# Optimization experiments

Measured on AMD Instinct MI355X. Metric: run time of the kernel, lower is better.

The kernel has to match this reference:

```python
import jax, jax.numpy as jnp
import numpy as np

H = 97
IN = 9
N_NODES = 100000
N_EDGES = 800000
N_GRAPHS = 4096
N_LAYERS = 7
N_STEPS = 7
BN_EPS = 1e-5


def setup_inputs() -> dict:
    key = jax.random.key(0)
    ks = iter(jax.random.split(key, 40))
    sc = 0.1  # param init scale
    inp = {}
    inp['x'] = jax.random.normal(next(ks), (N_NODES, IN), jnp.float32)
    inp['edge_index'] = jax.random.randint(next(ks), (2, N_EDGES), 0, N_NODES, jnp.int32)
    inp['batch'] = jnp.sort(jax.random.randint(next(ks), (N_NODES,), 0, N_GRAPHS, jnp.int32))
    inp['num_graphs'] = N_GRAPHS
    inp['lin1_W'] = jax.random.normal(next(ks), (IN, H), jnp.float32) * sc
    inp['lin1_b'] = jax.random.normal(next(ks), (H,), jnp.float32) * sc
    for nm in ['Wk', 'Wq', 'Wv', 'Ws']:
        inp['conv_' + nm] = jax.random.normal(next(ks), (N_LAYERS, H, H), jnp.float32) * sc
    for nm in ['bk', 'bq', 'bv', 'bs']:
        inp['conv_' + nm] = jax.random.normal(next(ks), (N_LAYERS, H), jnp.float32) * sc
    inp['gru_Wih'] = jax.random.normal(next(ks), (N_LAYERS, H, 3 * H), jnp.float32) * sc
    inp['gru_Whh'] = jax.random.normal(next(ks), (N_LAYERS, H, 3 * H), jnp.float32) * sc
    inp['gru_bih'] = jax.random.normal(next(ks), (N_LAYERS, 3 * H), jnp.float32) * sc
    inp['gru_bhh'] = jax.random.normal(next(ks), (N_LAYERS, 3 * H), jnp.float32) * sc
    inp['bn_gamma'] = jnp.ones((N_LAYERS - 1, H), jnp.float32)
    inp['bn_beta'] = jnp.zeros((N_LAYERS - 1, H), jnp.float32)
    inp['bn_mean'] = jnp.zeros((N_LAYERS - 1, H), jnp.float32)
    inp['bn_var'] = jnp.ones((N_LAYERS - 1, H), jnp.float32)
    inp['gat_W'] = jax.random.normal(next(ks), (H, H), jnp.float32) * sc
    inp['gat_asrc'] = jax.random.normal(next(ks), (H,), jnp.float32) * sc
    inp['gat_adst'] = jax.random.normal(next(ks), (H,), jnp.float32) * sc
    inp['gat_b'] = jax.random.normal(next(ks), (H,), jnp.float32) * sc
    inp['molgru_Wih'] = jax.random.normal(next(ks), (H, 3 * H), jnp.float32) * sc
    inp['molgru_Whh'] = jax.random.normal(next(ks), (H, 3 * H), jnp.float32) * sc
    inp['molgru_bih'] = jax.random.normal(next(ks), (3 * H,), jnp.float32) * sc
    inp['molgru_bhh'] = jax.random.normal(next(ks), (3 * H,), jnp.float32) * sc
    inp['lin2_W'] = jax.random.normal(next(ks), (H, 1), jnp.float32) * sc
    inp['lin2_b'] = jax.random.normal(next(ks), (1,), jnp.float32) * sc
    return inp


def _gru(xin, h, Wih, Whh, bih, bhh):
    gi = xin @ Wih + bih  # [N, 3H]
    gh = h @ Whh + bhh
    ir, iz, inn = jnp.split(gi, 3, axis=-1)
    hr, hz, hn = jnp.split(gh, 3, axis=-1)
    r = jax.nn.sigmoid(ir + hr)
    z = jax.nn.sigmoid(iz + hz)
    n = jnp.tanh(inn + r * hn)
    return (1.0 - z) * n + z * h


def _resgated(x, src, dst, Wk, bk, Wq, bq, Wv, bv, Ws, bs, n_nodes):
    # PyG ResGatedGraphConv: out_i = Ws x_i + sum_j sigmoid(Wk x_i + Wq x_j) * (Wv x_j)
    k = x @ Wk + bk
    q = x @ Wq + bq
    v = x @ Wv + bv
    msg = jax.nn.sigmoid(k[dst] + q[src]) * v[src]  # [E, H]
    agg = jax.ops.segment_sum(msg, dst, num_segments=n_nodes)
    return agg + (x @ Ws + bs)


def _forward(x, lin1_W, lin1_b, conv_Wk, conv_bk, conv_Wq, conv_bq, conv_Wv, conv_bv,
             conv_Ws, conv_bs, gru_Wih, gru_Whh, gru_bih, gru_bhh,
             bn_gamma, bn_beta, bn_mean, bn_var,
             gat_W, gat_asrc, gat_adst, gat_b,
             molgru_Wih, molgru_Whh, molgru_bih, molgru_bhh,
             lin2_W, lin2_b, edge_index, batch, num_graphs):
    src, dst = edge_index[0], edge_index[1]
    n_nodes = x.shape[0]
    x = jax.nn.leaky_relu(x @ lin1_W + lin1_b, 0.01)
    # layer 0 (gate_conv + gru)
    h = jax.nn.elu(_resgated(x, src, dst, conv_Wk[0], conv_bk[0], conv_Wq[0], conv_bq[0],
                             conv_Wv[0], conv_bv[0], conv_Ws[0], conv_bs[0], n_nodes))
    x = jax.nn.relu(_gru(h, x, gru_Wih[0], gru_Whh[0], gru_bih[0], gru_bhh[0]))
    # layers 1..6 with eval-mode BatchNorm (dropout inactive in eval)
    for l in range(1, N_LAYERS):
        h = jax.nn.elu(_resgated(x, src, dst, conv_Wk[l], conv_bk[l], conv_Wq[l], conv_bq[l],
                                 conv_Wv[l], conv_bv[l], conv_Ws[l], conv_bs[l], n_nodes))
        b = l - 1
        h = (h - bn_mean[b]) * (bn_gamma[b] / jnp.sqrt(bn_var[b] + BN_EPS)) + bn_beta[b]
        x = jax.nn.relu(_gru(h, x, gru_Wih[l], gru_Whh[l], gru_bih[l], gru_bhh[l]))
    # molecule readout: global_add_pool then bipartite GAT (heads=1) over node->graph edges
    out = jax.nn.relu(jax.ops.segment_sum(x, batch, num_segments=num_graphs))  # [G, H]
    xs = x @ gat_W          # source projections, fixed over timesteps
    a_s = xs @ gat_asrc     # [N]
    for _ in range(N_STEPS):
        a_d = (out @ gat_W) @ gat_adst  # [G]
        alpha = jax.nn.leaky_relu(a_s + a_d[batch], 0.01)  # one score per node-edge
        m = jax.ops.segment_max(alpha, batch, num_segments=num_graphs)
        m = jnp.where(jnp.isfinite(m), m, 0.0)
        e = jnp.exp(alpha - m[batch])
        s = jax.ops.segment_sum(e, batch, num_segments=num_graphs)
        w = e / s[batch]  # segment softmax over each graph's nodes
        hg = jax.ops.segment_sum(w[:, None] * xs, batch, num_segments=num_graphs) + gat_b
        h = jax.nn.elu(hg)
        out = jax.nn.relu(_gru(h, out, molgru_Wih, molgru_Whh, molgru_bih, molgru_bhh))
    return out @ lin2_W + lin2_b  # [G, 1]


def reference(x, edge_index, batch, num_graphs, lin1_W, lin1_b, conv_Wk, conv_bk, conv_Wq,
              conv_bq, conv_Wv, conv_bv, conv_Ws, conv_bs, gru_Wih, gru_Whh, gru_bih, gru_bhh,
              bn_gamma, bn_beta, bn_mean, bn_var, gat_W, gat_asrc, gat_adst, gat_b,
              molgru_Wih, molgru_Whh, molgru_bih, molgru_bhh, lin2_W, lin2_b):
    return _forward(x, lin1_W, lin1_b, conv_Wk, conv_bk, conv_Wq, conv_bq, conv_Wv, conv_bv,
                    conv_Ws, conv_bs, gru_Wih, gru_Whh, gru_bih, gru_bhh,
                    bn_gamma, bn_beta, bn_mean, bn_var,
                    gat_W, gat_asrc, gat_adst, gat_b,
                    molgru_Wih, molgru_Whh, molgru_bih, molgru_bhh,
                    lin2_W, lin2_b, edge_index, batch, num_graphs)
```

## Files before the change

kernel.cpp:

```cpp
#include <hip/hip_runtime.h>

#define NN 100000
#define NNP 100032
#define NE 800000
#define NG 4096
#define HH 97
#define HP 128
#define NB 391

typedef unsigned short u16;
typedef unsigned int u32;
typedef __attribute__((ext_vector_type(8))) short short8v;
typedef __attribute__((ext_vector_type(4))) float f32x4;

__device__ __forceinline__ float sigm_(float x){ return 1.f/(1.f+__expf(-x)); }
__device__ __forceinline__ float lrelu01_(float x){ return x>0.f? x : 0.01f*x; }
__device__ __forceinline__ float tanh_(float t){ float e2=__expf(2.f*t); return 1.f-2.f/(e2+1.f); }
__device__ __forceinline__ float b2f(u16 u){ union{u32 i; float f;} t; t.i=(u32)u<<16; return t.f; }
__device__ __forceinline__ u16 f2b(float x){ union{float f; u32 i;} t; t.f=x; u32 r=t.i+0x7FFFu+((t.i>>16)&1u); return (u16)(r>>16); }

__device__ __forceinline__ f32x4 mfma16(short8v a, short8v b, f32x4 c){
  return __builtin_amdgcn_mfma_f32_16x16x32_bf16(a, b, c, 0, 0, 0);
}

__global__ void k_pack_convw(const float* __restrict__ Wk, const float* __restrict__ Wq,
                             const float* __restrict__ Wv, const float* __restrict__ Ws,
                             u16* __restrict__ out){
  int idx = blockIdx.x*256 + threadIdx.x;
  if (idx >= 7*2*4*32*512) return;
  int e = idx & 7, lane = (idx>>3) & 63, t = (idx>>9) & 31;
  int ks = (idx>>14) & 3, term = (idx>>16) & 1, l = idx>>17;
  int k = ks*32 + (lane>>4)*8 + e;
  int n = t*16 + (lane & 15);
  int m = n>>7, h = n & 127;
  float val = 0.f;
  if (k < HH && h < HH){
    const float* W = (m==0)? Wk : (m==1)? Wq : (m==2)? Wv : Ws;
    val = W[l*9409 + k*97 + h];
  }
  u16 hi = f2b(val);
  out[idx] = (term==0)? hi : f2b(val - b2f(hi));
}

__global__ void k_pack_gruw(const float* __restrict__ gih, const float* __restrict__ ghh,
                            const float* __restrict__ mih, const float* __restrict__ mhh,
                            u16* __restrict__ out){
  int idx = blockIdx.x*256 + threadIdx.x;
  if (idx >= 8*2*2*4*24*512) return;
  int e = idx & 7, lane = (idx>>3) & 63;
  int r1 = idx>>9;
  int t = r1 % 24, r2 = r1 / 24;
  int ks = r2 & 3, mt = (r2>>2) & 3, set = r2>>4;
  int mat = mt>>1, term = mt & 1;
  int k = ks*32 + (lane>>4)*8 + e;
  int n = t*16 + (lane & 15);
  int j = n>>7, g = n & 127;
  float val = 0.f;
  if (k < HH && g < HH){
    const float* src = (set < 7)? ((mat==0)? gih + (size_t)set*28227 : ghh + (size_t)set*28227)
                                : ((mat==0)? mih : mhh);
    val = src[k*291 + j*97 + g];
  }
  u16 hi = f2b(val);
  out[idx] = (term==0)? hi : f2b(val - b2f(hi));
}

__global__ void k_pack_gatw(const float* __restrict__ gatW, u16* __restrict__ out){
  int idx = blockIdx.x*256 + threadIdx.x;
  if (idx >= 2*4*8*512) return;
  int e = idx & 7, lane = (idx>>3) & 63, t = (idx>>9) & 7;
  int ks = (idx>>12) & 3, term = idx>>14;
  int k = ks*32 + (lane>>4)*8 + e;
  int h = t*16 + (lane & 15);
  float val = (k < HH && h < HH)? gatW[k*97 + h] : 0.f;
  u16 hi = f2b(val);
  out[idx] = (term==0)? hi : f2b(val - b2f(hi));
}

__global__ void k_pack_w96(const float* __restrict__ Wk, const float* __restrict__ Wq,
                           const float* __restrict__ Wv, const float* __restrict__ Ws,
                           const float* __restrict__ gih, const float* __restrict__ ghh,
                           const float* __restrict__ mih, const float* __restrict__ mhh,
                           float* __restrict__ out){
  int idx = blockIdx.x*256 + threadIdx.x;
  if (idx < 7*512){
    int l = idx >> 9, c = idx & 511;
    int m = c >> 7, h = c & 127;
    float v = 0.f;
    if (h < HH){
      const float* W = (m==0)? Wk : (m==1)? Wq : (m==2)? Wv : Ws;
      v = W[l*9409 + 96*97 + h];
    }
    out[idx] = v;
  } else if (idx < 7*512 + 8*384){
    int r = idx - 7*512;
    int set = r / 384, n = r % 384;
    int j = n >> 7, g = n & 127;
    float v = 0.f;
    if (g < HH){
      const float* srcp = (set < 7)? gih + (size_t)set*28227 : mih;
      v = srcp[96*291 + j*97 + g];
    }
    out[idx] = v;
  } else if (idx < 7*512 + 16*384){
    int r = idx - 7*512 - 8*384;
    int set = r / 384, n = r % 384;
    int j = n >> 7, g = n & 127;
    float v = 0.f;
    if (g < HH){
      const float* srcp = (set < 7)? ghh + (size_t)set*28227 : mhh;
      v = srcp[96*291 + j*97 + g];
    }
    out[idx] = v;
  }
}

__global__ void k_pack_convb(const float* __restrict__ bk, const float* __restrict__ bq,
                             const float* __restrict__ bv, const float* __restrict__ bs,
                             float* __restrict__ out){
  int idx = blockIdx.x*256 + threadIdx.x;
  if (idx >= 7*512) return;
  int l = idx >> 9, c = idx & 511;
  int m = c >> 7, h = c & 127;
  float v = 0.f;
  if (h < HH){
    const float* B = (m==0)? bk : (m==1)? bq : (m==2)? bv : bs;
    v = B[l*97 + h];
  }
  out[idx] = v;
}

__global__ void k_pack_grub(const float* __restrict__ gbi, const float* __restrict__ gbh,
                            const float* __restrict__ mbi, const float* __restrict__ mbh,
                            float* __restrict__ obi, float* __restrict__ obh){
  int idx = blockIdx.x*256 + threadIdx.x;
  if (idx >= 8*384) return;
  int set = idx / 384, n = idx % 384;
  int j = n>>7, g = n & 127;
  float vi = 0.f, vh = 0.f;
  if (g < HH){
    const float* si = (set < 7)? gbi + set*291 : mbi;
    const float* sh = (set < 7)? gbh + set*291 : mbh;
    vi = si[j*97 + g];
    vh = sh[j*97 + g];
  }
  obi[idx] = vi; obh[idx] = vh;
}

__global__ void k_pack_misc(const float* __restrict__ gatW, const float* __restrict__ asrc,
                            const float* __restrict__ adst, const float* __restrict__ gatb,
                            const float* __restrict__ l2W, float* __restrict__ out){
  int idx = blockIdx.x*256 + threadIdx.x;
  if (idx < 16384){
    int k = idx >> 7, h = idx & 127;
    out[idx] = (k < HH && h < HH)? gatW[k*97 + h] : 0.f;
  } else if (idx < 16512){
    int h = idx - 16384; out[idx] = (h < HH)? asrc[h] : 0.f;
  } else if (idx < 16640){
    int h = idx - 16512; out[idx] = (h < HH)? adst[h] : 0.f;
  } else if (idx < 16768){
    int h = idx - 16640; out[idx] = (h < HH)? gatb[h] : 0.f;
  } else if (idx < 16896){
    int h = idx - 16768; out[idx] = (h < HH)? l2W[h] : 0.f;
  } else if (idx < 17408){
    out[idx] = 0.f;
  }
}

__global__ void k_seg(const int* __restrict__ batch, int* __restrict__ seg){
  int g = blockIdx.x*blockDim.x + threadIdx.x;
  if (g > NG) return;
  int lo = 0, hi = NN;
  while (lo < hi){ int mid = (lo+hi) >> 1; if (batch[mid] < g) lo = mid+1; else hi = mid; }
  seg[g] = lo;
}

__global__ void k_hist(const int* __restrict__ dst, int* __restrict__ cnt){
  int e = blockIdx.x*256 + threadIdx.x;
  if (e < NE) atomicAdd(&cnt[dst[e]], 1);
}

__global__ void k_scan_blk(const int* __restrict__ cnt, int* __restrict__ offs,
                           int* __restrict__ bsum){
  __shared__ int s[256];
  int b = blockIdx.x, t = threadIdx.x, i = b*256 + t;
  int v = (i < NN)? cnt[i] : 0;
  s[t] = v; __syncthreads();
  #pragma unroll
  for (int off = 1; off < 256; off <<= 1){
    int tmp = (t >= off)? s[t-off] : 0;
    __syncthreads();
    s[t] += tmp;
    __syncthreads();
  }
  if (i < NN) offs[i] = s[t] - v;
  if (t == 255) bsum[b] = s[255];
}

__global__ void k_scan_top(int* __restrict__ bsum){
  __shared__ int s[512];
  int t = threadIdx.x;
  int v = (t < NB)? bsum[t] : 0;
  s[t] = v; __syncthreads();
  #pragma unroll
  for (int off = 1; off < 512; off <<= 1){
    int tmp = (t >= off)? s[t-off] : 0;
    __syncthreads();
    s[t] += tmp;
    __syncthreads();
  }
  if (t < NB) bsum[t] = s[t] - v;
}

__global__ void k_scan_add(int* __restrict__ offs, const int* __restrict__ bsum,
                           int* __restrict__ cur){
  int b = blockIdx.x, t = threadIdx.x, i = b*256 + t;
  if (i < NN){ int o = offs[i] + bsum[b]; offs[i] = o; cur[i] = o; }
  if (i == 0) offs[NN] = NE;
}

__global__ void k_scatter(const int* __restrict__ src, const int* __restrict__ dst,
                          int* __restrict__ cur, int* __restrict__ eidx){
  int e = blockIdx.x*256 + threadIdx.x;
  if (e >= NE) return;
  int pos = atomicAdd(&cur[dst[e]], 1);
  eidx[pos] = src[e];
}

__global__ __launch_bounds__(256) void k_lin1(const float* __restrict__ x,
    const float* __restrict__ W, const float* __restrict__ b, u16* __restrict__ X0){
  int idx = blockIdx.x*256 + threadIdx.x;
  int n = idx >> 7, c = idx & 127;
  float v = 0.f;
  if (n < NN && c < HH){
    v = b[c];
    #pragma unroll
    for (int k = 0; k < 9; ++k) v += x[n*9 + k]*W[k*HH + c];
    v = lrelu01_(v);
  }
  X0[(size_t)n*HP + c] = f2b(v);
}

__global__ __launch_bounds__(256) void k_conv_mfma(const u16* __restrict__ X,
    const u16* __restrict__ WCF_l, const float* __restrict__ biasp,
    const float* __restrict__ W96C, u16* __restrict__ KQV, float* __restrict__ S){
  int tid = threadIdx.x;
  int w = tid >> 6, lane = tid & 63;
  int lm = lane & 15, ls = lane >> 4;
  int m0 = blockIdx.x*64;
  f32x4 acc[4][8] = {};
  for (int ks = 0; ks < 3; ++ks){
    short8v aX[4];
    #pragma unroll
    for (int rb = 0; rb < 4; ++rb)
      aX[rb] = *(const short8v*)(X + (size_t)(m0 + rb*16 + lm)*HP + ks*32 + ls*8);
    short8v wf[8][2];
    #pragma unroll
    for (int t = 0; t < 8; ++t){
      int tg = w*8 + t;
      wf[t][0] = *(const short8v*)(WCF_l + (((size_t)(0*4 + ks)*32 + tg)*64 + lane)*8);
      wf[t][1] = *(const short8v*)(WCF_l + (((size_t)(1*4 + ks)*32 + tg)*64 + lane)*8);
    }
    #pragma unroll
    for (int t = 0; t < 8; ++t)
      #pragma unroll
      for (int rb = 0; rb < 4; ++rb){
        acc[rb][t] = mfma16(aX[rb], wf[t][0], acc[rb][t]);
        acc[rb][t] = mfma16(aX[rb], wf[t][1], acc[rb][t]);
      }
  }
  float x96[4][4];
  #pragma unroll
  for (int rb = 0; rb < 4; ++rb)
    #pragma unroll
    for (int r = 0; r < 4; ++r)
      x96[rb][r] = b2f(X[(size_t)(m0 + rb*16 + ls*4 + r)*HP + 96]);
  #pragma unroll
  for (int t = 0; t < 8; ++t){
    int c = t*16 + lm;
    int col = w*128 + c;
    float bv = biasp[col];
    float w96 = W96C[col];
    #pragma unroll
    for (int rb = 0; rb < 4; ++rb)
      #pragma unroll
      for (int r = 0; r < 4; ++r){
        int row = m0 + rb*16 + ls*4 + r;
        float v = acc[rb][t][r] + bv + x96[rb][r]*w96;
        if (w < 3) KQV[(size_t)row*384 + w*128 + c] = f2b(v);
        else       S[(size_t)row*HP + c] = v;
      }
  }
}

__global__ __launch_bounds__(256) void k_gru_mfma(const float* __restrict__ Hin,
    const u16* __restrict__ Xin, const u16* __restrict__ WGF_set,
    const float* __restrict__ bihp, const float* __restrict__ bhhp,
    const float* __restrict__ W96I, const float* __restrict__ W96H,
    u16* __restrict__ Xout){
  int tid = threadIdx.x;
  int w = tid >> 6, lane = tid & 63;
  int lm = lane & 15, ls = lane >> 4;
  int m0 = blockIdx.x*32;
  f32x4 agi[2][2][3] = {};
  f32x4 agh[2][2][3] = {};
  for (int ks = 0; ks < 3; ++ks){
    short8v aX[2], aSh[2], aSl[2];
    #pragma unroll
    for (int rb = 0; rb < 2; ++rb){
      int row = m0 + rb*16 + lm;
      aX[rb] = *(const short8v*)(Xin + (size_t)row*HP + ks*32 + ls*8);
      const float* sp = Hin + (size_t)row*HP + ks*32 + ls*8;
      float sv[8];
      *(float4*)&sv[0] = *(const float4*)sp;
      *(float4*)&sv[4] = *(const float4*)(sp + 4);
      short8v vh, vl;
      #pragma unroll
      for (int e = 0; e < 8; ++e){
        u16 hb = f2b(sv[e]);
        vh[e] = (short)hb;
        vl[e] = (short)f2b(sv[e] - b2f(hb));
      }
      aSh[rb] = vh; aSl[rb] = vl;
    }
    #pragma unroll
    for (int b = 0; b < 2; ++b){
      short8v fI[3][2], fH[3][2];
      #pragma unroll
      for (int j = 0; j < 3; ++j){
        int t = j*8 + 2*w + b;
        fI[j][0] = *(const short8v*)(WGF_set + (((size_t)(0*4 + ks)*24 + t)*64 + lane)*8);
        fI[j][1] = *(const short8v*)(WGF_set + (((size_t)(1*4 + ks)*24 + t)*64 + lane)*8);
        fH[j][0] = *(const short8v*)(WGF_set + (((size_t)(2*4 + ks)*24 + t)*64 + lane)*8);
        fH[j][1] = *(const short8v*)(WGF_set + (((size_t)(3*4 + ks)*24 + t)*64 + lane)*8);
      }
      #pragma unroll
      for (int j = 0; j < 3; ++j)
        #pragma unroll
        for (int rb = 0; rb < 2; ++rb){
          agi[rb][b][j] = mfma16(aSh[rb], fI[j][0], agi[rb][b][j]);
          agi[rb][b][j] = mfma16(aSh[rb], fI[j][1], agi[rb][b][j]);
          agi[rb][b][j] = mfma16(aSl[rb], fI[j][0], agi[rb][b][j]);
          agh[rb][b][j] = mfma16(aX[rb], fH[j][0], agh[rb][b][j]);
          agh[rb][b][j] = mfma16(aX[rb], fH[j][1], agh[rb][b][j]);
        }
    }
  }
  float s96[2][4], x96[2][4];
  #pragma unroll
  for (int rb = 0; rb < 2; ++rb)
    #pragma unroll
    for (int r = 0; r < 4; ++r){
      int row = m0 + rb*16 + ls*4 + r;
      s96[rb][r] = Hin[(size_t)row*HP + 96];
      x96[rb][r] = b2f(Xin[(size_t)row*HP + 96]);
    }
  #pragma unroll
  for (int b = 0; b < 2; ++b){
    int g = (2*w + b)*16 + lm;
    float bi0 = bihp[g], bi1 = bihp[128+g], bi2 = bihp[256+g];
    float bh0 = bhhp[g], bh1 = bhhp[128+g], bh2 = bhhp[256+g];
    float wi0 = W96I[g], wi1 = W96I[128+g], wi2 = W96I[256+g];
    float wh0 = W96H[g], wh1 = W96H[128+g], wh2 = W96H[256+g];
    #pragma unroll
    for (int rb = 0; rb < 2; ++rb)
      #pragma unroll
      for (int r = 0; r < 4; ++r){
        int row = m0 + rb*16 + ls*4 + r;
        float ir = agi[rb][b][0][r] + bi0 + s96[rb][r]*wi0;
        float iz = agi[rb][b][1][r] + bi1 + s96[rb][r]*wi1;
        float in_ = agi[rb][b][2][r] + bi2 + s96[rb][r]*wi2;
        float hr = agh[rb][b][0][r] + bh0 + x96[rb][r]*wh0;
        float hz = agh[rb][b][1][r] + bh1 + x96[rb][r]*wh1;
        float hn = agh[rb][b][2][r] + bh2 + x96[rb][r]*wh2;
        float rr = sigm_(ir + hr);
        float zz = sigm_(iz + hz);
        float nn2 = tanh_(in_ + rr*hn);
        float xo = b2f(Xin[(size_t)row*HP + g]);
        float v = (1.f - zz)*nn2 + zz*xo;
        Xout[(size_t)row*HP + g] = f2b(fmaxf(v, 0.f));
      }
  }
}

__global__ __launch_bounds__(256) void k_xs_mfma(const u16* __restrict__ X,
    const u16* __restrict__ GATF, u16* __restrict__ XS){
  int tid = threadIdx.x;
  int w = tid >> 6, lane = tid & 63;
  int lm = lane & 15, ls = lane >> 4;
  int m0 = blockIdx.x*32;
  f32x4 acc[2][2] = {};
  for (int ks = 0; ks < 4; ++ks){
    short8v aX[2];
    #pragma unroll
    for (int rb = 0; rb < 2; ++rb){
      int row = m0 + rb*16 + lm;
      aX[rb] = *(const short8v*)(X + (size_t)row*HP + ks*32 + ls*8);
    }
    #pragma unroll
    for (int b = 0; b < 2; ++b){
      int t = 2*w + b;
      short8v bh = *(const short8v*)(GATF + (((size_t)(0*4 + ks)*8 + t)*64 + lane)*8);
      short8v bl = *(const short8v*)(GATF + (((size_t)(1*4 + ks)*8 + t)*64 + lane)*8);
      #pragma unroll
      for (int rb = 0; rb < 2; ++rb){
        acc[rb][b] = mfma16(aX[rb], bh, acc[rb][b]);
        acc[rb][b] = mfma16(aX[rb], bl, acc[rb][b]);
      }
    }
  }
  #pragma unroll
  for (int b = 0; b < 2; ++b){
    int c = (2*w + b)*16 + lm;
    #pragma unroll
    for (int rb = 0; rb < 2; ++rb)
      #pragma unroll
      for (int r = 0; r < 4; ++r){
        int row = m0 + rb*16 + ls*4 + r;
        XS[(size_t)row*HP + c] = f2b(acc[rb][b][r]);
      }
  }
}

__global__ __launch_bounds__(256) void k_agg(const u16* __restrict__ kqv,
    const int* __restrict__ offs, const int* __restrict__ eidx,
    float* __restrict__ S, const float* __restrict__ gamma, const float* __restrict__ beta,
    const float* __restrict__ mean, const float* __restrict__ var, int layer){
  int n = blockIdx.x*4 + (threadIdx.x >> 6);
  if (n >= NN) return;
  int lane = threadIdx.x & 63;
  int c2 = lane*2;
  int lo = offs[n], hi = offs[n+1];
  ushort2 kk = *(const ushort2*)(kqv + (size_t)n*384 + c2);
  float k0 = b2f(kk.x), k1 = b2f(kk.y);
  float a0 = 0.f, a1 = 0.f;
  int i = lo;
  for (; i + 4 <= hi; i += 4){
    int s0 = eidx[i], s1 = eidx[i+1], s2 = eidx[i+2], s3 = eidx[i+3];
    const u16* q0 = kqv + (size_t)s0*384 + 128 + c2;
    const u16* q1 = kqv + (size_t)s1*384 + 128 + c2;
    const u16* q2 = kqv + (size_t)s2*384 + 128 + c2;
    const u16* q3 = kqv + (size_t)s3*384 + 128 + c2;
    ushort2 qa = *(const ushort2*)q0, va = *(const ushort2*)(q0 + 128);
    ushort2 qb = *(const ushort2*)q1, vb = *(const ushort2*)(q1 + 128);
    ushort2 qc = *(const ushort2*)q2, vc = *(const ushort2*)(q2 + 128);
    ushort2 qd = *(const ushort2*)q3, vd = *(const ushort2*)(q3 + 128);
    a0 += b2f(va.x)*sigm_(k0 + b2f(qa.x)); a1 += b2f(va.y)*sigm_(k1 + b2f(qa.y));
    a0 += b2f(vb.x)*sigm_(k0 + b2f(qb.x)); a1 += b2f(vb.y)*sigm_(k1 + b2f(qb.y));
    a0 += b2f(vc.x)*sigm_(k0 + b2f(qc.x)); a1 += b2f(vc.y)*sigm_(k1 + b2f(qc.y));
    a0 += b2f(vd.x)*sigm_(k0 + b2f(qd.x)); a1 += b2f(vd.y)*sigm_(k1 + b2f(qd.y));
  }
  for (; i < hi; ++i){
    int s = eidx[i];
    const u16* qb0 = kqv + (size_t)s*384 + 128 + c2;
    ushort2 qq = *(const ushort2*)qb0;
    ushort2 vv = *(const ushort2*)(qb0 + 128);
    a0 += b2f(vv.x)*sigm_(k0 + b2f(qq.x));
    a1 += b2f(vv.y)*sigm_(k1 + b2f(qq.y));
  }
  float* sp = S + (size_t)n*HP + c2;
  float2 sr = *(float2*)sp;
  float v0 = sr.x + a0, v1 = sr.y + a1;
  v0 = v0 > 0.f ? v0 : (__expf(v0) - 1.f);
  v1 = v1 > 0.f ? v1 : (__expf(v1) - 1.f);
  if (layer > 0){
    int b0 = (layer-1)*97 + c2;
    if (c2 < HH){ float sc = gamma[b0]*rsqrtf(var[b0] + 1e-5f); v0 = (v0 - mean[b0])*sc + beta[b0]; }
    if (c2+1 < HH){ float sc = gamma[b0+1]*rsqrtf(var[b0+1] + 1e-5f); v1 = (v1 - mean[b0+1])*sc + beta[b0+1]; }
  }
  if (c2 >= HH)   v0 = 0.f;
  if (c2+1 >= HH) v1 = 0.f;
  *(float2*)sp = make_float2(v0, v1);
}

__global__ __launch_bounds__(128) void k_pool(const int* __restrict__ seg,
    const u16* __restrict__ x, u16* __restrict__ out){
  int g = blockIdx.x, tid = threadIdx.x;
  int lo = seg[g], hi = seg[g+1];
  float acc = 0.f;
  for (int n = lo; n < hi; ++n) acc += b2f(x[(size_t)n*HP + tid]);
  out[(size_t)g*HP + tid] = f2b(fmaxf(acc, 0.f));
}

__global__ __launch_bounds__(256) void k_as(const u16* __restrict__ xs,
    const float* __restrict__ asrcp, float* __restrict__ a_s){
  int t = blockIdx.x*256 + threadIdx.x;
  int n = t >> 6, lane = t & 63;
  float v = b2f(xs[(size_t)n*HP + lane])*asrcp[lane]
          + b2f(xs[(size_t)n*HP + 64 + lane])*asrcp[64 + lane];
  #pragma unroll
  for (int o = 32; o > 0; o >>= 1) v += __shfl_down(v, o);
  if (lane == 0) a_s[n] = v;
}

__global__ __launch_bounds__(128) void k_ad(const u16* __restrict__ out,
    const float* __restrict__ gatwp, const float* __restrict__ adstp, float* __restrict__ ad){
  int g = blockIdx.x, tid = threadIdx.x;
  __shared__ float so[HP];
  __shared__ float red[2];
  so[tid] = b2f(out[(size_t)g*HP + tid]);
  __syncthreads();
  float p = 0.f;
  #pragma unroll 4
  for (int k = 0; k < HP; ++k) p += so[k]*gatwp[k*HP + tid];
  float v = p * adstp[tid];
  #pragma unroll
  for (int o = 32; o > 0; o >>= 1) v += __shfl_down(v, o);
  if ((tid & 63) == 0) red[tid >> 6] = v;
  __syncthreads();
  if (tid == 0) ad[g] = red[0] + red[1];
}

#define ACAP 2048
__global__ __launch_bounds__(128) void k_attn(const int* __restrict__ seg,
    const float* __restrict__ a_s, const float* __restrict__ a_d,
    const u16* __restrict__ xs, const float* __restrict__ gbp, float* __restrict__ hg){
  int g = blockIdx.x, tid = threadIdx.x;
  int lo = seg[g], hi = seg[g+1], cnt = hi - lo;
  float ad = a_d[g];
  __shared__ float sa[ACAP];
  __shared__ float red[2];
  float mloc = -3.4e38f;
  for (int i = tid; i < cnt; i += 128){
    float al = lrelu01_(a_s[lo+i] + ad);
    if (i < ACAP) sa[i] = al;
    mloc = fmaxf(mloc, al);
  }
  #pragma unroll
  for (int o = 32; o > 0; o >>= 1) mloc = fmaxf(mloc, __shfl_down(mloc, o));
  if ((tid & 63) == 0) red[tid >> 6] = mloc;
  __syncthreads();
  float mm = fmaxf(red[0], red[1]);
  __syncthreads();
  float sloc = 0.f;
  for (int i = tid; i < cnt; i += 128){
    float al = (i < ACAP)? sa[i] : lrelu01_(a_s[lo+i] + ad);
    float e = __expf(al - mm);
    if (i < ACAP) sa[i] = e;
    sloc += e;
  }
  #pragma unroll
  for (int o = 32; o > 0; o >>= 1) sloc += __shfl_down(sloc, o);
  if ((tid & 63) == 0) red[tid >> 6] = sloc;
  __syncthreads();
  float ss = red[0] + red[1];
  float inv = (cnt > 0 && ss != 0.f)? 1.f/ss : 0.f;
  __syncthreads();
  float accv = 0.f;
  for (int i = 0; i < cnt; ++i){
    float e = (i < ACAP)? sa[i] : __expf(lrelu01_(a_s[lo+i] + ad) - mm);
    accv += (e*inv) * b2f(xs[(size_t)(lo+i)*HP + tid]);
  }
  float hgv = accv + gbp[tid];
  hg[(size_t)g*HP + tid] = hgv > 0.f ? hgv : (__expf(hgv) - 1.f);
}

__global__ __launch_bounds__(64) void k_final(const u16* __restrict__ out,
    const float* __restrict__ w2p, const float* __restrict__ l2b, float* __restrict__ y){
  int g = blockIdx.x, lane = threadIdx.x;
  float v = b2f(out[(size_t)g*HP + lane])*w2p[lane]
          + b2f(out[(size_t)g*HP + 64 + lane])*w2p[64 + lane];
  #pragma unroll
  for (int o = 32; o > 0; o >>= 1) v += __shfl_down(v, o);
  if (lane == 0) y[g] = v + l2b[0];
}

extern "C" void kernel_launch(void* const* d_in, const int* in_sizes, int n_in,
                              void* d_out, int out_size, void* d_ws, size_t ws_size,
                              hipStream_t stream){
  const float* x_in  = (const float*)d_in[0];
  const int*   ei    = (const int*)d_in[1];
  const int*   batch = (const int*)d_in[2];
  const float* lin1W = (const float*)d_in[4];
  const float* lin1b = (const float*)d_in[5];
  const float* cWk = (const float*)d_in[6];
  const float* cWq = (const float*)d_in[7];
  const float* cWv = (const float*)d_in[8];
  const float* cWs = (const float*)d_in[9];
  const float* cbk = (const float*)d_in[10];
  const float* cbq = (const float*)d_in[11];
  const float* cbv = (const float*)d_in[12];
  const float* cbs = (const float*)d_in[13];
  const float* gWih = (const float*)d_in[14];
  const float* gWhh = (const float*)d_in[15];
  const float* gbih = (const float*)d_in[16];
  const float* gbhh = (const float*)d_in[17];
  const float* bng = (const float*)d_in[18];
  const float* bnb = (const float*)d_in[19];
  const float* bnm = (const float*)d_in[20];
  const float* bnv = (const float*)d_in[21];
  const float* gatW  = (const float*)d_in[22];
  const float* gasrc = (const float*)d_in[23];
  const float* gadst = (const float*)d_in[24];
  const float* gatb  = (const float*)d_in[25];
  const float* mWih = (const float*)d_in[26];
  const float* mWhh = (const float*)d_in[27];
  const float* mbih = (const float*)d_in[28];
  const float* mbhh = (const float*)d_in[29];
  const float* l2W = (const float*)d_in[30];
  const float* l2b = (const float*)d_in[31];
  const int* src = ei;
  const int* dst = ei + NE;

  char* base = (char*)d_ws;
  size_t off = 0;
  auto alloc = [&](size_t nbytes)->char*{
    char* p = base + off; off = (off + nbytes + 255) & ~(size_t)255; return p; };

  u16*  WCF  = (u16*)alloc((size_t)7*2*4*32*512*2);
  u16*  WGF  = (u16*)alloc((size_t)8*2*2*4*24*512*2);
  u16*  GATF = (u16*)alloc((size_t)2*4*8*512*2);
  float* W96  = (float*)alloc((size_t)(7*512 + 16*384)*4);
  float* BCONVP = (float*)alloc(7*512*4);
  float* BIHP   = (float*)alloc(8*384*4);
  float* BHHP   = (float*)alloc(8*384*4);
  float* GATWP  = (float*)alloc(17408*4);
  float* ASRCP = GATWP + 16384;
  float* ADSTP = GATWP + 16512;
  float* GBP   = GATWP + 16640;
  float* W2P   = GATWP + 16768;
  u16*  X0  = (u16*)alloc((size_t)NNP*HP*2);
  u16*  X1  = (u16*)alloc((size_t)NNP*HP*2);
  u16*  KQV = (u16*)alloc((size_t)NNP*384*2);
  float* S  = (float*)alloc((size_t)NNP*HP*4);
  float* AS_ = (float*)alloc((size_t)NN*4);
  float* AD_ = (float*)alloc((size_t)NG*4);
  u16*  OUTA = (u16*)alloc((size_t)NG*HP*2);
  u16*  OUTB = (u16*)alloc((size_t)NG*HP*2);
  float* HG  = (float*)alloc((size_t)NG*HP*4);
  int*  SEG  = (int*)alloc((size_t)(NG+1)*4);
  int*  CNT  = (int*)alloc((size_t)NN*4);
  int*  OFFS = (int*)alloc((size_t)(NN+1)*4);
  int*  CUR  = (int*)alloc((size_t)NN*4);
  int*  EIDX = (int*)alloc((size_t)NE*4);
  int*  BSUM = (int*)alloc((size_t)NB*4);

  float* W96C = W96;
  float* W96I = W96 + 7*512;
  float* W96H = W96 + 7*512 + 8*384;

  if (ws_size < off){
    hipMemsetAsync(d_out, 0, (size_t)out_size*sizeof(float), stream);
    return;
  }

  k_pack_convw<<<(7*2*4*32*512+255)/256,256,0,stream>>>(cWk,cWq,cWv,cWs,WCF);
  k_pack_gruw<<<(8*2*2*4*24*512+255)/256,256,0,stream>>>(gWih,gWhh,mWih,mWhh,WGF);
  k_pack_gatw<<<(2*4*8*512+255)/256,256,0,stream>>>(gatW,GATF);
  k_pack_w96<<<(7*512+16*384+255)/256,256,0,stream>>>(cWk,cWq,cWv,cWs,gWih,gWhh,mWih,mWhh,W96);
  k_pack_convb<<<(7*512+255)/256,256,0,stream>>>(cbk,cbq,cbv,cbs,BCONVP);
  k_pack_grub<<<(8*384+255)/256,256,0,stream>>>(gbih,gbhh,mbih,mbhh,BIHP,BHHP);
  k_pack_misc<<<68,256,0,stream>>>(gatW,gasrc,gadst,gatb,l2W,GATWP);
  k_lin1<<<(NNP*HP)/256,256,0,stream>>>(x_in,lin1W,lin1b,X0);
  k_seg<<<(NG+1+255)/256,256,0,stream>>>(batch,SEG);

  hipMemsetAsync(CNT, 0, (size_t)NN*4, stream);
  k_hist<<<(NE+255)/256,256,0,stream>>>(dst, CNT);
  k_scan_blk<<<NB,256,0,stream>>>(CNT, OFFS, BSUM);
  k_scan_top<<<1,512,0,stream>>>(BSUM);
  k_scan_add<<<NB,256,0,stream>>>(OFFS, BSUM, CUR);
  k_scatter<<<(NE+255)/256,256,0,stream>>>(src, dst, CUR, EIDX);

  for (int l = 0; l < 7; ++l){
    u16* Xin  = (l & 1)? X1 : X0;
    u16* Xout = (l & 1)? X0 : X1;
    k_conv_mfma<<<NNP/64,256,0,stream>>>(Xin, WCF + (size_t)l*131072, BCONVP + l*512,
                                         W96C + l*512, KQV, S);
    k_agg<<<(NN+3)/4,256,0,stream>>>(KQV, OFFS, EIDX, S, bng, bnb, bnm, bnv, l);
    k_gru_mfma<<<NNP/32,256,0,stream>>>(S, Xin, WGF + (size_t)l*196608,
                                        BIHP + l*384, BHHP + l*384,
                                        W96I + l*384, W96H + l*384, Xout);
  }
  u16* XF = X1;

  k_pool<<<NG,128,0,stream>>>(SEG, XF, OUTA);
  u16* XS = KQV;
  k_xs_mfma<<<NNP/32,256,0,stream>>>(XF, GATF, XS);
  k_as<<<(NN*64)/256,256,0,stream>>>(XS, ASRCP, AS_);

  u16* cur = OUTA; u16* nxt = OUTB;
  for (int s = 0; s < 7; ++s){
    k_ad<<<NG,128,0,stream>>>(cur, GATWP, ADSTP, AD_);
    k_attn<<<NG,128,0,stream>>>(SEG, AS_, AD_, XS, GBP, HG);
    k_gru_mfma<<<NG/32,256,0,stream>>>(HG, cur, WGF + (size_t)7*196608,
                                       BIHP + 7*384, BHHP + 7*384,
                                       W96I + 7*384, W96H + 7*384, nxt);
    u16* t = cur; cur = nxt; nxt = t;
  }
  k_final<<<NG,64,0,stream>>>(cur, W2P, l2b, (float*)d_out);
}
```

Baseline: 2.447 ms.

## Store S as bf16 hi/lo split, repack weights compactly, widen GRU row tile

The fp32 S and HG buffers become pairs of bf16 hi/lo arrays, produced in the conv, agg and attention kernels, so the GRU kernel loads ready-made MFMA operands instead of converting fp32 each time. The conv and GRU weight fragments are repacked so each wave reads contiguous chunks, and the unused fourth k-slice is dropped, which shrinks the weight buffers. The GRU kernel now processes 64 rows per block instead of 32, reusing each weight fragment over more rows at the cost of more accumulator registers. Traffic for S stays the same size, but k_agg now does extra split and merge arithmetic.

```diff
diff --git a/kernel.cpp b/kernel.cpp
--- a/kernel.cpp
+++ b/kernel.cpp
@@ -8,6 +8,9 @@
 #define HP 128
 #define NB 391
 
+#define WGF_SET_STRIDE 147456
+#define WCF_LAYER_STRIDE 98304
+
 typedef unsigned short u16;
 typedef unsigned int u32;
 typedef __attribute__((ext_vector_type(8))) short short8v;
@@ -27,11 +30,15 @@
                              const float* __restrict__ Wv, const float* __restrict__ Ws,
                              u16* __restrict__ out){
   int idx = blockIdx.x*256 + threadIdx.x;
-  if (idx >= 7*2*4*32*512) return;
-  int e = idx & 7, lane = (idx>>3) & 63, t = (idx>>9) & 31;
-  int ks = (idx>>14) & 3, term = (idx>>16) & 1, l = idx>>17;
+  if (idx >= 7*4*8*3*2*512) return;
+  int e = idx & 7, lane = (idx>>3) & 63;
+  int r = idx >> 9;
+  int term = r & 1; r >>= 1;
+  int ks = r % 3; r /= 3;
+  int t = r & 7; r >>= 3;
+  int w = r & 3; int l = r >> 2;
   int k = ks*32 + (lane>>4)*8 + e;
-  int n = t*16 + (lane & 15);
+  int n = (w*8 + t)*16 + (lane & 15);
   int m = n>>7, h = n & 127;
   float val = 0.f;
   if (k < HH && h < HH){
@@ -46,23 +53,25 @@
                             const float* __restrict__ mih, const float* __restrict__ mhh,
                             u16* __restrict__ out){
   int idx = blockIdx.x*256 + threadIdx.x;
-  if (idx >= 8*2*2*4*24*512) return;
+  if (idx >= 8*8*3*3*4*512) return;
   int e = idx & 7, lane = (idx>>3) & 63;
-  int r1 = idx>>9;
-  int t = r1 % 24, r2 = r1 / 24;
-  int ks = r2 & 3, mt = (r2>>2) & 3, set = r2>>4;
-  int mat = mt>>1, term = mt & 1;
+  int r = idx >> 9;
+  int mat = r & 3; r >>= 2;
+  int ks = r % 3; r /= 3;
+  int j = r % 3; r /= 3;
+  int bt = r & 7; int set = r >> 3;
   int k = ks*32 + (lane>>4)*8 + e;
-  int n = t*16 + (lane & 15);
-  int j = n>>7, g = n & 127;
+  int n = (j*8 + bt)*16 + (lane & 15);
+  int jg = n>>7, g = n & 127;
   float val = 0.f;
   if (k < HH && g < HH){
-    const float* src = (set < 7)? ((mat==0)? gih + (size_t)set*28227 : ghh + (size_t)set*28227)
-                                : ((mat==0)? mih : mhh);
-    val = src[k*291 + j*97 + g];
+    const float* srcp;
+    if (mat < 2) srcp = (set < 7)? gih + (size_t)set*28227 : mih;
+    else         srcp = (set < 7)? ghh + (size_t)set*28227 : mhh;
+    val = srcp[k*291 + jg*97 + g];
   }
   u16 hi = f2b(val);
-  out[idx] = (term==0)? hi : f2b(val - b2f(hi));
+  out[idx] = ((mat & 1)==0)? hi : f2b(val - b2f(hi));
 }
 
 __global__ void k_pack_gatw(const float* __restrict__ gatW, u16* __restrict__ out){
@@ -243,12 +252,15 @@
 
 __global__ __launch_bounds__(256) void k_conv_mfma(const u16* __restrict__ X,
     const u16* __restrict__ WCF_l, const float* __restrict__ biasp,
-    const float* __restrict__ W96C, u16* __restrict__ KQV, float* __restrict__ S){
+    const float* __restrict__ W96C, u16* __restrict__ KQV,
+    u16* __restrict__ Sh, u16* __restrict__ Sl){
   int tid = threadIdx.x;
-  int w = tid >> 6, lane = tid & 63;
+  int w = __builtin_amdgcn_readfirstlane(tid >> 6);
+  int lane = tid & 63;
   int lm = lane & 15, ls = lane >> 4;
   int m0 = blockIdx.x*64;
   f32x4 acc[4][8] = {};
+  const u16* pw = WCF_l + (size_t)w*24576 + lane*8;
   for (int ks = 0; ks < 3; ++ks){
     short8v aX[4];
     #pragma unroll
@@ -257,9 +269,9 @@
     short8v wf[8][2];
     #pragma unroll
     for (int t = 0; t < 8; ++t){
-      int tg = w*8 + t;
-      wf[t][0] = *(const short8v*)(WCF_l + (((size_t)(0*4 + ks)*32 + tg)*64 + lane)*8);
-      wf[t][1] = *(const short8v*)(WCF_l + (((size_t)(1*4 + ks)*32 + tg)*64 + lane)*8);
+      const u16* q = pw + ((t*3 + ks) << 10);
+      wf[t][0] = *(const short8v*)(q);
+      wf[t][1] = *(const short8v*)(q + 512);
     }
     #pragma unroll
     for (int t = 0; t < 8; ++t)
@@ -288,72 +300,69 @@
         int row = m0 + rb*16 + ls*4 + r;
         float v = acc[rb][t][r] + bv + x96[rb][r]*w96;
         if (w < 3) KQV[(size_t)row*384 + w*128 + c] = f2b(v);
-        else       S[(size_t)row*HP + c] = v;
+        else {
+          u16 hb = f2b(v);
+          Sh[(size_t)row*HP + c] = hb;
+          Sl[(size_t)row*HP + c] = f2b(v - b2f(hb));
+        }
       }
   }
 }
 
-__global__ __launch_bounds__(256) void k_gru_mfma(const float* __restrict__ Hin,
-    const u16* __restrict__ Xin, const u16* __restrict__ WGF_set,
+__global__ __launch_bounds__(256) void k_gru_mfma(const u16* __restrict__ Sh_,
+    const u16* __restrict__ Sl_, const u16* __restrict__ Xin,
+    const u16* __restrict__ WGF_set,
     const float* __restrict__ bihp, const float* __restrict__ bhhp,
     const float* __restrict__ W96I, const float* __restrict__ W96H,
     u16* __restrict__ Xout){
   int tid = threadIdx.x;
-  int w = tid >> 6, lane = tid & 63;
+  int w = __builtin_amdgcn_readfirstlane(tid >> 6);
+  int lane = tid & 63;
   int lm = lane & 15, ls = lane >> 4;
-  int m0 = blockIdx.x*32;
-  f32x4 agi[2][2][3] = {};
-  f32x4 agh[2][2][3] = {};
+  int m0 = blockIdx.x*64;
+  f32x4 agi[4][2][3] = {};
+  f32x4 agh[4][2][3] = {};
   for (int ks = 0; ks < 3; ++ks){
-    short8v aX[2], aSh[2], aSl[2];
-    #pragma unroll
-    for (int rb = 0; rb < 2; ++rb){
-      int row = m0 + rb*16 + lm;
-      aX[rb] = *(const short8v*)(Xin + (size_t)row*HP + ks*32 + ls*8);
-      const float* sp = Hin + (size_t)row*HP + ks*32 + ls*8;
-      float sv[8];
-      *(float4*)&sv[0] = *(const float4*)sp;
-      *(float4*)&sv[4] = *(const float4*)(sp + 4);
-      short8v vh, vl;
-      #pragma unroll
-      for (int e = 0; e < 8; ++e){
-        u16 hb = f2b(sv[e]);
-        vh[e] = (short)hb;
-        vl[e] = (short)f2b(sv[e] - b2f(hb));
-      }
-      aSh[rb] = vh; aSl[rb] = vl;
+    short8v aX[4], aSh[4], aSl[4];
+    #pragma unroll
+    for (int rb = 0; rb < 4; ++rb){
+      size_t off = (size_t)(m0 + rb*16 + lm)*HP + ks*32 + ls*8;
+      aX[rb]  = *(const short8v*)(Xin + off);
+      aSh[rb] = *(const short8v*)(Sh_ + off);
+      aSl[rb] = *(const short8v*)(Sl_ + off);
     }
     #pragma unroll
     for (int b = 0; b < 2; ++b){
-      short8v fI[3][2], fH[3][2];
+      const u16* pb = WGF_set + (size_t)(2*w + b)*18432 + lane*8;
+      short8v fIh[3], fIl[3], fHh[3], fHl[3];
       #pragma unroll
       for (int j = 0; j < 3; ++j){
-        int t = j*8 + 2*w + b;
-        fI[j][0] = *(const short8v*)(WGF_set + (((size_t)(0*4 + ks)*24 + t)*64 + lane)*8);
-        fI[j][1] = *(const short8v*)(WGF_set + (((size_t)(1*4 + ks)*24 + t)*64 + lane)*8);
-        fH[j][0] = *(const short8v*)(WGF_set + (((size_t)(2*4 + ks)*24 + t)*64 + lane)*8);
-        fH[j][1] = *(const short8v*)(WGF_set + (((size_t)(3*4 + ks)*24 + t)*64 + lane)*8);
+        const u16* q = pb + ((j*3 + ks) << 11);
+        fIh[j] = *(const short8v*)(q);
+        fIl[j] = *(const short8v*)(q + 512);
+        fHh[j] = *(const short8v*)(q + 1024);
+        fHl[j] = *(const short8v*)(q + 1536);
       }
       #pragma unroll
       for (int j = 0; j < 3; ++j)
         #pragma unroll
-        for (int rb = 0; rb < 2; ++rb){
-          agi[rb][b][j] = mfma16(aSh[rb], fI[j][0], agi[rb][b][j]);
-          agi[rb][b][j] = mfma16(aSh[rb], fI[j][1], agi[rb][b][j]);
-          agi[rb][b][j] = mfma16(aSl[rb], fI[j][0], agi[rb][b][j]);
-          agh[rb][b][j] = mfma16(aX[rb], fH[j][0], agh[rb][b][j]);
-          agh[rb][b][j] = mfma16(aX[rb], fH[j][1], agh[rb][b][j]);
+        for (int rb = 0; rb < 4; ++rb){
+          agi[rb][b][j] = mfma16(aSh[rb], fIh[j], agi[rb][b][j]);
+          agi[rb][b][j] = mfma16(aSh[rb], fIl[j], agi[rb][b][j]);
+          agi[rb][b][j] = mfma16(aSl[rb], fIh[j], agi[rb][b][j]);
+          agh[rb][b][j] = mfma16(aX[rb], fHh[j], agh[rb][b][j]);
+          agh[rb][b][j] = mfma16(aX[rb], fHl[j], agh[rb][b][j]);
         }
     }
   }
-  float s96[2][4], x96[2][4];
-  #pragma unroll
-  for (int rb = 0; rb < 2; ++rb)
+  float s96[4][4], x96[4][4];
+  #pragma unroll
+  for (int rb = 0; rb < 4; ++rb)
     #pragma unroll
     for (int r = 0; r < 4; ++r){
-      int row = m0 + rb*16 + ls*4 + r;
-      s96[rb][r] = Hin[(size_t)row*HP + 96];
-      x96[rb][r] = b2f(Xin[(size_t)row*HP + 96]);
+      size_t o96 = (size_t)(m0 + rb*16 + ls*4 + r)*HP + 96;
+      s96[rb][r] = b2f(Sh_[o96]) + b2f(Sl_[o96]);
+      x96[rb][r] = b2f(Xin[o96]);
     }
   #pragma unroll
   for (int b = 0; b < 2; ++b){
@@ -363,7 +372,7 @@
     float wi0 = W96I[g], wi1 = W96I[128+g], wi2 = W96I[256+g];
     float wh0 = W96H[g], wh1 = W96H[128+g], wh2 = W96H[256+g];
     #pragma unroll
-    for (int rb = 0; rb < 2; ++rb)
+    for (int rb = 0; rb < 4; ++rb)
       #pragma unroll
       for (int r = 0; r < 4; ++r){
         int row = m0 + rb*16 + ls*4 + r;
@@ -424,7 +433,8 @@
 
 __global__ __launch_bounds__(256) void k_agg(const u16* __restrict__ kqv,
     const int* __restrict__ offs, const int* __restrict__ eidx,
-    float* __restrict__ S, const float* __restrict__ gamma, const float* __restrict__ beta,
+    u16* __restrict__ Sh, u16* __restrict__ Sl,
+    const float* __restrict__ gamma, const float* __restrict__ beta,
     const float* __restrict__ mean, const float* __restrict__ var, int layer){
   int n = blockIdx.x*4 + (threadIdx.x >> 6);
   if (n >= NN) return;
@@ -458,9 +468,12 @@
     a0 += b2f(vv.x)*sigm_(k0 + b2f(qq.x));
     a1 += b2f(vv.y)*sigm_(k1 + b2f(qq.y));
   }
-  float* sp = S + (size_t)n*HP + c2;
-  float2 sr = *(float2*)sp;
-  float v0 = sr.x + a0, v1 = sr.y + a1;
+  u16* shp = Sh + (size_t)n*HP + c2;
+  u16* slp = Sl + (size_t)n*HP + c2;
+  ushort2 sh2 = *(const ushort2*)shp;
+  ushort2 sl2 = *(const ushort2*)slp;
+  float v0 = b2f(sh2.x) + b2f(sl2.x) + a0;
+  float v1 = b2f(sh2.y) + b2f(sl2.y) + a1;
   v0 = v0 > 0.f ? v0 : (__expf(v0) - 1.f);
   v1 = v1 > 0.f ? v1 : (__expf(v1) - 1.f);
   if (layer > 0){
@@ -470,7 +483,9 @@
   }
   if (c2 >= HH)   v0 = 0.f;
   if (c2+1 >= HH) v1 = 0.f;
-  *(float2*)sp = make_float2(v0, v1);
+  u16 h0 = f2b(v0), h1 = f2b(v1);
+  *(ushort2*)shp = make_ushort2(h0, h1);
+  *(ushort2*)slp = make_ushort2(f2b(v0 - b2f(h0)), f2b(v1 - b2f(h1)));
 }
 
 __global__ __launch_bounds__(128) void k_pool(const int* __restrict__ seg,
@@ -514,7 +529,8 @@
 #define ACAP 2048
 __global__ __launch_bounds__(128) void k_attn(const int* __restrict__ seg,
     const float* __restrict__ a_s, const float* __restrict__ a_d,
-    const u16* __restrict__ xs, const float* __restrict__ gbp, float* __restrict__ hg){
+    const u16* __restrict__ xs, const float* __restrict__ gbp,
+    u16* __restrict__ hgh, u16* __restrict__ hgl){
   int g = blockIdx.x, tid = threadIdx.x;
   int lo = seg[g], hi = seg[g+1], cnt = hi - lo;
   float ad = a_d[g];
@@ -552,7 +568,10 @@
     accv += (e*inv) * b2f(xs[(size_t)(lo+i)*HP + tid]);
   }
   float hgv = accv + gbp[tid];
-  hg[(size_t)g*HP + tid] = hgv > 0.f ? hgv : (__expf(hgv) - 1.f);
+  hgv = hgv > 0.f ? hgv : (__expf(hgv) - 1.f);
+  u16 hb = f2b(hgv);
+  hgh[(size_t)g*HP + tid] = hb;
+  hgl[(size_t)g*HP + tid] = f2b(hgv - b2f(hb));
 }
 
 __global__ __launch_bounds__(64) void k_final(const u16* __restrict__ out,
@@ -607,8 +626,8 @@
   auto alloc = [&](size_t nbytes)->char*{
     char* p = base + off; off = (off + nbytes + 255) & ~(size_t)255; return p; };
 
-  u16*  WCF  = (u16*)alloc((size_t)7*2*4*32*512*2);
-  u16*  WGF  = (u16*)alloc((size_t)8*2*2*4*24*512*2);
+  u16*  WCF  = (u16*)alloc((size_t)7*WCF_LAYER_STRIDE*2);
+  u16*  WGF  = (u16*)alloc((size_t)8*WGF_SET_STRIDE*2);
   u16*  GATF = (u16*)alloc((size_t)2*4*8*512*2);
   float* W96  = (float*)alloc((size_t)(7*512 + 16*384)*4);
   float* BCONVP = (float*)alloc(7*512*4);
@@ -622,12 +641,14 @@
   u16*  X0  = (u16*)alloc((size_t)NNP*HP*2);
   u16*  X1  = (u16*)alloc((size_t)NNP*HP*2);
   u16*  KQV = (u16*)alloc((size_t)NNP*384*2);
-  float* S  = (float*)alloc((size_t)NNP*HP*4);
+  u16*  Sh  = (u16*)alloc((size_t)NNP*HP*2);
+  u16*  Sl  = (u16*)alloc((size_t)NNP*HP*2);
   float* AS_ = (float*)alloc((size_t)NN*4);
   float* AD_ = (float*)alloc((size_t)NG*4);
   u16*  OUTA = (u16*)alloc((size_t)NG*HP*2);
   u16*  OUTB = (u16*)alloc((size_t)NG*HP*2);
-  float* HG  = (float*)alloc((size_t)NG*HP*4);
+  u16*  HGH  = (u16*)alloc((size_t)NG*HP*2);
+  u16*  HGL  = (u16*)alloc((size_t)NG*HP*2);
   int*  SEG  = (int*)alloc((size_t)(NG+1)*4);
   int*  CNT  = (int*)alloc((size_t)NN*4);
   int*  OFFS = (int*)alloc((size_t)(NN+1)*4);
@@ -644,8 +665,8 @@
     return;
   }
 
-  k_pack_convw<<<(7*2*4*32*512+255)/256,256,0,stream>>>(cWk,cWq,cWv,cWs,WCF);
-  k_pack_gruw<<<(8*2*2*4*24*512+255)/256,256,0,stream>>>(gWih,gWhh,mWih,mWhh,WGF);
+  k_pack_convw<<<(7*WCF_LAYER_STRIDE)/256,256,0,stream>>>(cWk,cWq,cWv,cWs,WCF);
+  k_pack_gruw<<<(8*WGF_SET_STRIDE)/256,256,0,stream>>>(gWih,gWhh,mWih,mWhh,WGF);
   k_pack_gatw<<<(2*4*8*512+255)/256,256,0,stream>>>(gatW,GATF);
   k_pack_w96<<<(7*512+16*384+255)/256,256,0,stream>>>(cWk,cWq,cWv,cWs,gWih,gWhh,mWih,mWhh,W96);
   k_pack_convb<<<(7*512+255)/256,256,0,stream>>>(cbk,cbq,cbv,cbs,BCONVP);
@@ -664,10 +685,10 @@
   for (int l = 0; l < 7; ++l){
     u16* Xin  = (l & 1)? X1 : X0;
     u16* Xout = (l & 1)? X0 : X1;
-    k_conv_mfma<<<NNP/64,256,0,stream>>>(Xin, WCF + (size_t)l*131072, BCONVP + l*512,
-                                         W96C + l*512, KQV, S);
-    k_agg<<<(NN+3)/4,256,0,stream>>>(KQV, OFFS, EIDX, S, bng, bnb, bnm, bnv, l);
-    k_gru_mfma<<<NNP/32,256,0,stream>>>(S, Xin, WGF + (size_t)l*196608,
+    k_conv_mfma<<<NNP/64,256,0,stream>>>(Xin, WCF + (size_t)l*WCF_LAYER_STRIDE,
+                                         BCONVP + l*512, W96C + l*512, KQV, Sh, Sl);
+    k_agg<<<(NN+3)/4,256,0,stream>>>(KQV, OFFS, EIDX, Sh, Sl, bng, bnb, bnm, bnv, l);
+    k_gru_mfma<<<NNP/64,256,0,stream>>>(Sh, Sl, Xin, WGF + (size_t)l*WGF_SET_STRIDE,
                                         BIHP + l*384, BHHP + l*384,
                                         W96I + l*384, W96H + l*384, Xout);
   }
@@ -681,8 +702,8 @@
   u16* cur = OUTA; u16* nxt = OUTB;
   for (int s = 0; s < 7; ++s){
     k_ad<<<NG,128,0,stream>>>(cur, GATWP, ADSTP, AD_);
-    k_attn<<<NG,128,0,stream>>>(SEG, AS_, AD_, XS, GBP, HG);
-    k_gru_mfma<<<NG/32,256,0,stream>>>(HG, cur, WGF + (size_t)7*196608,
+    k_attn<<<NG,128,0,stream>>>(SEG, AS_, AD_, XS, GBP, HGH, HGL);
+    k_gru_mfma<<<NG/64,256,0,stream>>>(HGH, HGL, cur, WGF + (size_t)7*WGF_SET_STRIDE,
                                        BIHP + 7*384, BHHP + 7*384,
                                        W96I + 7*384, W96H + 7*384, nxt);
     u16* t = cur; cur = nxt; nxt = t;
```

Result: slower. 2.613 ms (+6.8%).
